# Optimization experiments

Hardware: AMD Instinct MI355X
Metric: run time of the kernel (lower is better)

Reference implementation:

```python
import jax, jax.numpy as jnp
import numpy as np

B, NF, EMB = 2048, 32, 64
FEAT_MAP_DIM = [128, 128, 128]  # split_half=True, activation=None


def setup_inputs() -> dict:
    key = jax.random.key(0)
    ks = jax.random.split(key, 7)
    inp = jax.random.normal(ks[0], (B, NF, EMB), dtype=jnp.float32)
    # conv1d_i: in_channels = H_{i-1} * NF, out_channels = FEAT_MAP_DIM[i]
    # H_0 = NF = 32; H_1 = H_2 = 128 // 2 = 64 (split_half)
    in_chs = [NF * NF, (FEAT_MAP_DIM[0] // 2) * NF, (FEAT_MAP_DIM[1] // 2) * NF]
    params = {}
    for i, (ic, oc) in enumerate(zip(in_chs, FEAT_MAP_DIM)):
        bound = 1.0 / np.sqrt(ic)  # torch Conv1d default init range
        params[f"W{i}"] = jax.random.uniform(ks[1 + 2 * i], (oc, ic), jnp.float32, -bound, bound)
        params[f"b{i}"] = jax.random.uniform(ks[2 + 2 * i], (oc,), jnp.float32, -bound, bound)
    return {"inp": inp, **params}


def reference(inp, W0, b0, W1, b1, W2, b2):
    # CIN: h_k[b,o,e] = sum_{j,z} W_k[o, j*NF+z] * h_{k-1}[b,j,e] * inp[b,z,e] + b_k[o]
    # The torch code materializes the outer product then applies a 1x1 conv;
    # the fused triple einsum below computes identical math.
    nf = inp.shape[1]
    Ws, bs = [W0, W1, W2], [b0, b1, b2]
    h = inp
    outs = []
    n_layers = len(Ws)
    for i, (W, b) in enumerate(zip(Ws, bs)):
        O, Hj = W.shape[0], h.shape[1]
        Wr = W.reshape(O, Hj, nf)  # channel index c = j*nf + z
        nxt = jnp.einsum('bjk,bzk,ojz->bok', h, inp, Wr) + b[None, :, None]
        if i != n_layers - 1:  # split_half
            h, o = nxt[:, : O // 2], nxt[:, O // 2 :]
        else:
            o = nxt
        outs.append(o)
    out = jnp.concatenate(outs, axis=1)  # (B, 64+64+128, EMB)
    return jnp.sum(out, axis=2)  # (B, 256)
```

## Files before the change

### kernel.cpp

```cpp
#include <hip/hip_runtime.h>


typedef _Float16 f16;
typedef _Float16 f16x4 __attribute__((ext_vector_type(4)));
typedef _Float16 f16x8 __attribute__((ext_vector_type(8)));
typedef float f32x4 __attribute__((ext_vector_type(4)));
typedef float f32x16 __attribute__((ext_vector_type(16)));

#define HSTR 72
#define PBS  5120

__device__ __forceinline__ f32x16 zero16() {
    f32x16 v;
#pragma unroll
    for (int i = 0; i < 16; ++i) v[i] = 0.0f;
    return v;
}

__global__ void __launch_bounds__(256)
prep_frag(const float* __restrict__ W0, const float* __restrict__ W1,
          const float* __restrict__ W2, f16* __restrict__ dst)
{
    int g = (blockIdx.x * 256 + threadIdx.x) * 8;
    const float* src; int base, KK, rbase;
    if (g < 65536)       { src = W0; base = 0;      KK = 64;  rbase = 0;  }
    else if (g < 131072) { src = W0; base = 65536;  KK = 64;  rbase = 64; }
    else if (g < 262144) { src = W1; base = 131072; KK = 128; rbase = 0;  }
    else if (g < 393216) { src = W1; base = 262144; KK = 128; rbase = 64; }
    else                 { src = W2; base = 393216; KK = 128; rbase = 0;  }
    int local = g - base;
    int frag  = local >> 9;
    int lane  = (local >> 3) & 63;
    int kk    = frag % KK;
    int mc    = frag / KK;
    int row   = rbase + mc * 32 + (lane & 31);
    int col   = kk * 16 + (lane >> 5) * 8;
    int IC    = KK * 16;
    const float* s = src + (size_t)row * IC + col;
    f16x8 o;
#pragma unroll
    for (int i = 0; i < 8; ++i) o[i] = (f16)s[i];
    *(f16x8*)(dst + g) = o;
}

__device__ __forceinline__ void p_chunk(const f16* __restrict__ hrows,
                                        const f16x8 (&pB)[4],
                                        f16* __restrict__ pdst, int t, int q)
{
    f32x16 acc = zero16();
#pragma unroll
    for (int s = 0; s < 4; ++s) {
        f16x8 a = *(const f16x8*)(hrows + t * HSTR + s * 16 + q * 8);
        acc = __builtin_amdgcn_mfma_f32_32x32x16_f16(a, pB[s], acc, 0, 0, 0);
    }
#pragma unroll
    for (int r = 0; r < 16; ++r) {
        int row = (r & 3) + 8 * (r >> 2) + 4 * q;
        pdst[row * 32 + t] = (f16)acc[r];
    }
}

template <int HJ>
__device__ __forceinline__ void h_gemm4(const f16* __restrict__ Hf,
                                        const f16* __restrict__ h0,
                                        const f16* __restrict__ h1,
                                        int lane8, int t,
                                        const f16x8 (&ip)[2][2][2],
                                        f32x16 (&acc)[2][2])
{
    acc[0][0] = zero16(); acc[0][1] = zero16();
    acc[1][0] = zero16(); acc[1][1] = zero16();
    const f16* Wp = Hf + lane8;
    f16x8 wf[2][2];
    f16   sc[2][4];
#pragma unroll
    for (int ph = 0; ph < 2; ++ph) {
        wf[ph][0] = *(const f16x8*)(Wp + (ph * 2 + 0) * 512);
        wf[ph][1] = *(const f16x8*)(Wp + (ph * 2 + 1) * 512);
        sc[ph][0] = h0[ph * HSTR + t];
        sc[ph][1] = h0[ph * HSTR + 32 + t];
        sc[ph][2] = h1[ph * HSTR + t];
        sc[ph][3] = h1[ph * HSTR + 32 + t];
    }
    for (int jj = 0; jj < HJ; jj += 2) {
#pragma unroll
        for (int ph = 0; ph < 2; ++ph) {
            f16x8 w0 = wf[ph][0], w1 = wf[ph][1];
            f16 s00 = sc[ph][0], s01 = sc[ph][1];
            f16 s10 = sc[ph][2], s11 = sc[ph][3];
            int jn = jj + ph + 2;
            if (jn > HJ - 1) jn = HJ - 1;
            wf[ph][0] = *(const f16x8*)(Wp + (jn * 2 + 0) * 512);
            wf[ph][1] = *(const f16x8*)(Wp + (jn * 2 + 1) * 512);
            sc[ph][0] = h0[jn * HSTR + t];
            sc[ph][1] = h0[jn * HSTR + 32 + t];
            sc[ph][2] = h1[jn * HSTR + t];
            sc[ph][3] = h1[jn * HSTR + 32 + t];
            acc[0][0] = __builtin_amdgcn_mfma_f32_32x32x16_f16(w0, ip[0][0][0] * s00, acc[0][0], 0, 0, 0);
            acc[0][0] = __builtin_amdgcn_mfma_f32_32x32x16_f16(w1, ip[0][1][0] * s00, acc[0][0], 0, 0, 0);
            acc[0][1] = __builtin_amdgcn_mfma_f32_32x32x16_f16(w0, ip[0][0][1] * s01, acc[0][1], 0, 0, 0);
            acc[0][1] = __builtin_amdgcn_mfma_f32_32x32x16_f16(w1, ip[0][1][1] * s01, acc[0][1], 0, 0, 0);
            acc[1][0] = __builtin_amdgcn_mfma_f32_32x32x16_f16(w0, ip[1][0][0] * s10, acc[1][0], 0, 0, 0);
            acc[1][0] = __builtin_amdgcn_mfma_f32_32x32x16_f16(w1, ip[1][1][0] * s10, acc[1][0], 0, 0, 0);
            acc[1][1] = __builtin_amdgcn_mfma_f32_32x32x16_f16(w0, ip[1][0][1] * s11, acc[1][1], 0, 0, 0);
            acc[1][1] = __builtin_amdgcn_mfma_f32_32x32x16_f16(w1, ip[1][1][1] * s11, acc[1][1], 0, 0, 0);
        }
    }
}

__device__ __forceinline__ void load_bias(const float* __restrict__ bl,
                                          float (&bve)[16], int g, int q)
{
#pragma unroll
    for (int r = 0; r < 16; ++r)
        bve[r] = bl[g * 32 + (r & 3) + 8 * (r >> 2) + 4 * q];
}

__device__ __forceinline__ void epi4(const f32x16 (&acc)[2][2],
                                     f16* __restrict__ h0d, f16* __restrict__ h1d,
                                     const float (&bve)[16], int g, int t, int q)
{
#pragma unroll
    for (int r = 0; r < 16; ++r) {
        int row = g * 32 + (r & 3) + 8 * (r >> 2) + 4 * q;
        h0d[row * HSTR + t]      = (f16)(acc[0][0][r] + bve[r]);
        h0d[row * HSTR + 32 + t] = (f16)(acc[0][1][r] + bve[r]);
        h1d[row * HSTR + t]      = (f16)(acc[1][0][r] + bve[r]);
        h1d[row * HSTR + 32 + t] = (f16)(acc[1][1][r] + bve[r]);
    }
}

__global__ void __launch_bounds__(256, 2)
cin_h(const float* __restrict__ inp, const f16* __restrict__ Wf,
      f16* __restrict__ pW,
      const float* __restrict__ b0v, const float* __restrict__ b1v)
{
    __shared__ __attribute__((aligned(16))) f16 hL[4 * 64 * HSTR];

    const int tid   = threadIdx.x;
    const int w     = tid >> 6;
    const int lane  = tid & 63;
    const int t     = lane & 31;
    const int q     = lane >> 5;
    const int lane8 = lane * 8;
    const int bp    = w & 1;
    const int g     = w >> 1;
    const int b0i   = blockIdx.x * 4;

#pragma unroll
    for (int it = 0; it < 8; ++it) {
        int idx = it * 1024 + tid * 4;
        int b = idx >> 11, rem = idx & 2047;
        int z = rem >> 6, k = rem & 63;
        f32x4 v = *(const f32x4*)(inp + (size_t)(b0i + b) * 2048 + rem);
        f16x4 h4;
        h4[0] = (f16)v[0]; h4[1] = (f16)v[1]; h4[2] = (f16)v[2]; h4[3] = (f16)v[3];
        *(f16x4*)(hL + b * 64 * HSTR + z * HSTR + k) = h4;
    }
    __syncthreads();

    f16x8 ip[2][2][2];
#pragma unroll
    for (int b = 0; b < 2; ++b) {
        const f16* src = hL + (bp * 2 + b) * 64 * HSTR;
#pragma unroll
        for (int kq = 0; kq < 2; ++kq)
#pragma unroll
            for (int nh = 0; nh < 2; ++nh) {
                f16x8 v;
#pragma unroll
                for (int i = 0; i < 8; ++i)
                    v[i] = src[(kq * 16 + q * 8 + i) * HSTR + nh * 32 + t];
                ip[b][kq][nh] = v;
            }
    }
    f16x8 pB[4];
#pragma unroll
    for (int s = 0; s < 4; ++s)
        pB[s] = *(const f16x8*)(hL + w * 64 * HSTR + t * HSTR + s * 16 + q * 8);

    f16* pMy = pW + (size_t)(b0i + w) * PBS;
    const f16* H0 = Wf;
    const f16* H1 = Wf + 131072;
    f16* hA = hL + (bp * 2) * 64 * HSTR;
    f16* hB = hL + (bp * 2 + 1) * 64 * HSTR;
    f32x16 acc[2][2];
    float bve[16];

    p_chunk(hL + w * 64 * HSTR, pB, pMy, t, q);
    h_gemm4<32>(H0 + g * 64 * 512, hA, hB, lane8, t, ip, acc);
    load_bias(b0v, bve, g, q);
    __syncthreads();
    epi4(acc, hA, hB, bve, g, t, q);
    __syncthreads();

    p_chunk(hL + w * 64 * HSTR,             pB, pMy + 1024, t, q);
    p_chunk(hL + w * 64 * HSTR + 32 * HSTR, pB, pMy + 2048, t, q);
    h_gemm4<64>(H1 + g * 128 * 512, hA, hB, lane8, t, ip, acc);
    load_bias(b1v, bve, g, q);
    __syncthreads();
    epi4(acc, hA, hB, bve, g, t, q);
    __syncthreads();

    p_chunk(hL + w * 64 * HSTR,             pB, pMy + 3072, t, q);
    p_chunk(hL + w * 64 * HSTR + 32 * HSTR, pB, pMy + 4096, t, q);
}

template <int S>
__device__ __forceinline__ void o_tile(const f16* __restrict__ Of,
                                       const f16* __restrict__ pBase,
                                       const float* __restrict__ biasp,
                                       float* __restrict__ out,
                                       float* __restrict__ rP,
                                       int bg, int colbase, int tid)
{
    const int w = tid >> 6, lane = tid & 63, t = lane & 31, q = lane >> 5;
    const int lane8 = lane * 8;
    const int mi = w & 1, ki = w >> 1;
    const f16* Ap = Of + (size_t)(mi * 2 * S + ki * S) * 512 + lane8;
    const f16* Bp = pBase + (size_t)(bg * 32 + t) * PBS + ki * S * 16 + q * 8;

    f32x16 acc = zero16();
    f16x8 af[4], bf[4];
#pragma unroll
    for (int i = 0; i < 4; ++i) {
        af[i] = *(const f16x8*)(Ap + i * 512);
        bf[i] = *(const f16x8*)(Bp + i * 16);
    }
#pragma unroll 4
    for (int s = 0; s < S; ++s) {
        int idx = s & 3;
        f16x8 a = af[idx], b = bf[idx];
        int sn = s + 4 < S ? s + 4 : S - 1;
        af[idx] = *(const f16x8*)(Ap + sn * 512);
        bf[idx] = *(const f16x8*)(Bp + sn * 16);
        acc = __builtin_amdgcn_mfma_f32_32x32x16_f16(a, b, acc, 0, 0, 0);
    }
#pragma unroll
    for (int r = 0; r < 16; ++r) {
        int m = mi * 32 + (r & 3) + 8 * (r >> 2) + 4 * q;
        rP[(ki * 32 + t) * 64 + m] = acc[r];
    }
    __syncthreads();
#pragma unroll
    for (int it = 0; it < 2; ++it) {
        int idx4 = (it * 256 + tid) * 4;
        int n = idx4 >> 6, o = idx4 & 63;
        f32x4 v0 = *(const f32x4*)(rP + n * 64 + o);
        f32x4 v1 = *(const f32x4*)(rP + (32 + n) * 64 + o);
        f32x4 bb = *(const f32x4*)(biasp + o);
        f32x4 ov;
        ov[0] = v0[0] + v1[0] + 64.0f * bb[0];
        ov[1] = v0[1] + v1[1] + 64.0f * bb[1];
        ov[2] = v0[2] + v1[2] + 64.0f * bb[2];
        ov[3] = v0[3] + v1[3] + 64.0f * bb[3];
        *(f32x4*)(out + (size_t)(bg * 32 + n) * 256 + colbase + o) = ov;
    }
}

__global__ void __launch_bounds__(256, 2)
cin_out(const f16* __restrict__ Wf, const f16* __restrict__ pW,
        const float* __restrict__ b0v, const float* __restrict__ b1v,
        const float* __restrict__ b2v, float* __restrict__ out)
{
    __shared__ __attribute__((aligned(16))) float rP[2 * 32 * 64];
    const int tid = threadIdx.x;
    const int r  = blockIdx.x & 3;
    const int bg = blockIdx.x >> 2;
    if (r == 0)
        o_tile<32>(Wf + 65536,  pW,        b0v + 64, out, rP, bg, 0,   tid);
    else if (r == 1)
        o_tile<64>(Wf + 262144, pW + 1024, b1v + 64, out, rP, bg, 64,  tid);
    else if (r == 2)
        o_tile<64>(Wf + 393216, pW + 3072, b2v,      out, rP, bg, 128, tid);
    else
        o_tile<64>(Wf + 524288, pW + 3072, b2v + 64, out, rP, bg, 192, tid);
}

extern "C" void kernel_launch(void* const* d_in, const int* in_sizes, int n_in,
                              void* d_out, int out_size, void* d_ws, size_t ws_size,
                              hipStream_t stream)
{
    const float* inp = (const float*)d_in[0];
    const float* W0  = (const float*)d_in[1];
    const float* b0  = (const float*)d_in[2];
    const float* W1  = (const float*)d_in[3];
    const float* b1  = (const float*)d_in[4];
    const float* W2  = (const float*)d_in[5];
    const float* b2  = (const float*)d_in[6];
    float* out = (float*)d_out;

    f16* Wf = (f16*)d_ws;
    f16* pW = Wf + 655360;

    prep_frag<<<320, 256, 0, stream>>>(W0, W1, W2, Wf);
    cin_h<<<512, 256, 0, stream>>>(inp, Wf, pW, b0, b1);
    cin_out<<<256, 256, 0, stream>>>(Wf, pW, b0, b1, b2, out);
}
```

Baseline: 138.3 us.

## Stage weight fragments into LDS asynchronously and split output GEMM into 32-column tiles

The h-layer GEMM now streams weight fragments through a per-wave 4-slot LDS ring using global_load_lds with vmcnt waits, instead of register prefetch from global. This is meant to hide global latency and free registers. The output kernel is retiled so each block computes a 32-column slice with a 4-way K split across waves, doubling the grid to 512 blocks for better occupancy. It adds 32KB of shared memory per cin_h block, which may limit occupancy. The hand-written vmcnt counts must match the outstanding loads exactly, or the ring reads stale data.

```diff
diff --git a/kernel.cpp b/kernel.cpp
--- a/kernel.cpp
+++ b/kernel.cpp
@@ -16,6 +16,14 @@
     for (int i = 0; i < 16; ++i) v[i] = 0.0f;
     return v;
 }
+
+__device__ __forceinline__ void cp1k(const f16* g, f16* l) {
+    __builtin_amdgcn_global_load_lds(
+        (__attribute__((address_space(1))) void*)(unsigned long long)g,
+        (__attribute__((address_space(3))) void*)(unsigned int)(unsigned long long)l,
+        16, 0, 0);
+}
+#define WAITV(n) asm volatile("s_waitcnt vmcnt(" #n ")" ::: "memory")
 
 __global__ void __launch_bounds__(256)
 prep_frag(const float* __restrict__ W0, const float* __restrict__ W1,
@@ -60,52 +68,62 @@
     }
 }
 
+__device__ __forceinline__ void stage_j(const f16* __restrict__ Wg, int j,
+                                        f16* __restrict__ ring, int lane8)
+{
+    f16* slot = ring + (j & 3) * 1024;
+    const f16* gp = Wg + j * 1024 + lane8;
+    cp1k(gp, slot);
+    cp1k(gp + 512, slot + 512);
+}
+
+__device__ __forceinline__ void consume_j(const f16* __restrict__ ring, int j,
+                                          const f16* __restrict__ h0,
+                                          const f16* __restrict__ h1,
+                                          int lane8, int t,
+                                          const f16x8 (&ip)[2][2][2],
+                                          f32x16 (&acc)[2][2])
+{
+    const f16* slot = ring + (j & 3) * 1024;
+    f16x8 w0 = *(const f16x8*)(slot + lane8);
+    f16x8 w1 = *(const f16x8*)(slot + 512 + lane8);
+    f16 s00 = h0[j * HSTR + t];
+    f16 s01 = h0[j * HSTR + 32 + t];
+    f16 s10 = h1[j * HSTR + t];
+    f16 s11 = h1[j * HSTR + 32 + t];
+    acc[0][0] = __builtin_amdgcn_mfma_f32_32x32x16_f16(w0, ip[0][0][0] * s00, acc[0][0], 0, 0, 0);
+    acc[0][1] = __builtin_amdgcn_mfma_f32_32x32x16_f16(w0, ip[0][0][1] * s01, acc[0][1], 0, 0, 0);
+    acc[1][0] = __builtin_amdgcn_mfma_f32_32x32x16_f16(w0, ip[1][0][0] * s10, acc[1][0], 0, 0, 0);
+    acc[1][1] = __builtin_amdgcn_mfma_f32_32x32x16_f16(w0, ip[1][0][1] * s11, acc[1][1], 0, 0, 0);
+    acc[0][0] = __builtin_amdgcn_mfma_f32_32x32x16_f16(w1, ip[0][1][0] * s00, acc[0][0], 0, 0, 0);
+    acc[0][1] = __builtin_amdgcn_mfma_f32_32x32x16_f16(w1, ip[0][1][1] * s01, acc[0][1], 0, 0, 0);
+    acc[1][0] = __builtin_amdgcn_mfma_f32_32x32x16_f16(w1, ip[1][1][0] * s10, acc[1][0], 0, 0, 0);
+    acc[1][1] = __builtin_amdgcn_mfma_f32_32x32x16_f16(w1, ip[1][1][1] * s11, acc[1][1], 0, 0, 0);
+}
+
 template <int HJ>
-__device__ __forceinline__ void h_gemm4(const f16* __restrict__ Hf,
-                                        const f16* __restrict__ h0,
-                                        const f16* __restrict__ h1,
-                                        int lane8, int t,
-                                        const f16x8 (&ip)[2][2][2],
-                                        f32x16 (&acc)[2][2])
+__device__ __forceinline__ void h_gemm_async(const f16* __restrict__ Wg,
+                                             const f16* __restrict__ h0,
+                                             const f16* __restrict__ h1,
+                                             f16* __restrict__ ring,
+                                             int lane8, int t,
+                                             const f16x8 (&ip)[2][2][2],
+                                             f32x16 (&acc)[2][2])
 {
     acc[0][0] = zero16(); acc[0][1] = zero16();
     acc[1][0] = zero16(); acc[1][1] = zero16();
-    const f16* Wp = Hf + lane8;
-    f16x8 wf[2][2];
-    f16   sc[2][4];
-#pragma unroll
-    for (int ph = 0; ph < 2; ++ph) {
-        wf[ph][0] = *(const f16x8*)(Wp + (ph * 2 + 0) * 512);
-        wf[ph][1] = *(const f16x8*)(Wp + (ph * 2 + 1) * 512);
-        sc[ph][0] = h0[ph * HSTR + t];
-        sc[ph][1] = h0[ph * HSTR + 32 + t];
-        sc[ph][2] = h1[ph * HSTR + t];
-        sc[ph][3] = h1[ph * HSTR + 32 + t];
-    }
-    for (int jj = 0; jj < HJ; jj += 2) {
-#pragma unroll
-        for (int ph = 0; ph < 2; ++ph) {
-            f16x8 w0 = wf[ph][0], w1 = wf[ph][1];
-            f16 s00 = sc[ph][0], s01 = sc[ph][1];
-            f16 s10 = sc[ph][2], s11 = sc[ph][3];
-            int jn = jj + ph + 2;
-            if (jn > HJ - 1) jn = HJ - 1;
-            wf[ph][0] = *(const f16x8*)(Wp + (jn * 2 + 0) * 512);
-            wf[ph][1] = *(const f16x8*)(Wp + (jn * 2 + 1) * 512);
-            sc[ph][0] = h0[jn * HSTR + t];
-            sc[ph][1] = h0[jn * HSTR + 32 + t];
-            sc[ph][2] = h1[jn * HSTR + t];
-            sc[ph][3] = h1[jn * HSTR + 32 + t];
-            acc[0][0] = __builtin_amdgcn_mfma_f32_32x32x16_f16(w0, ip[0][0][0] * s00, acc[0][0], 0, 0, 0);
-            acc[0][0] = __builtin_amdgcn_mfma_f32_32x32x16_f16(w1, ip[0][1][0] * s00, acc[0][0], 0, 0, 0);
-            acc[0][1] = __builtin_amdgcn_mfma_f32_32x32x16_f16(w0, ip[0][0][1] * s01, acc[0][1], 0, 0, 0);
-            acc[0][1] = __builtin_amdgcn_mfma_f32_32x32x16_f16(w1, ip[0][1][1] * s01, acc[0][1], 0, 0, 0);
-            acc[1][0] = __builtin_amdgcn_mfma_f32_32x32x16_f16(w0, ip[1][0][0] * s10, acc[1][0], 0, 0, 0);
-            acc[1][0] = __builtin_amdgcn_mfma_f32_32x32x16_f16(w1, ip[1][1][0] * s10, acc[1][0], 0, 0, 0);
-            acc[1][1] = __builtin_amdgcn_mfma_f32_32x32x16_f16(w0, ip[1][0][1] * s11, acc[1][1], 0, 0, 0);
-            acc[1][1] = __builtin_amdgcn_mfma_f32_32x32x16_f16(w1, ip[1][1][1] * s11, acc[1][1], 0, 0, 0);
-        }
-    }
+    WAITV(0);
+    stage_j(Wg, 0, ring, lane8);
+    stage_j(Wg, 1, ring, lane8);
+    stage_j(Wg, 2, ring, lane8);
+    for (int j = 0; j < HJ - 3; ++j) {
+        WAITV(4);
+        stage_j(Wg, j + 3, ring, lane8);
+        consume_j(ring, j, h0, h1, lane8, t, ip, acc);
+    }
+    WAITV(4); consume_j(ring, HJ - 3, h0, h1, lane8, t, ip, acc);
+    WAITV(2); consume_j(ring, HJ - 2, h0, h1, lane8, t, ip, acc);
+    WAITV(0); consume_j(ring, HJ - 1, h0, h1, lane8, t, ip, acc);
 }
 
 __device__ __forceinline__ void load_bias(const float* __restrict__ bl,
@@ -136,6 +154,7 @@
       const float* __restrict__ b0v, const float* __restrict__ b1v)
 {
     __shared__ __attribute__((aligned(16))) f16 hL[4 * 64 * HSTR];
+    __shared__ __attribute__((aligned(16))) f16 ringS[4][4096];
 
     const int tid   = threadIdx.x;
     const int w     = tid >> 6;
@@ -146,6 +165,7 @@
     const int bp    = w & 1;
     const int g     = w >> 1;
     const int b0i   = blockIdx.x * 4;
+    f16* ring = ringS[w];
 
 #pragma unroll
     for (int it = 0; it < 8; ++it) {
@@ -188,7 +208,7 @@
     float bve[16];
 
     p_chunk(hL + w * 64 * HSTR, pB, pMy, t, q);
-    h_gemm4<32>(H0 + g * 64 * 512, hA, hB, lane8, t, ip, acc);
+    h_gemm_async<32>(H0 + g * 64 * 512, hA, hB, ring, lane8, t, ip, acc);
     load_bias(b0v, bve, g, q);
     __syncthreads();
     epi4(acc, hA, hB, bve, g, t, q);
@@ -196,7 +216,7 @@
 
     p_chunk(hL + w * 64 * HSTR,             pB, pMy + 1024, t, q);
     p_chunk(hL + w * 64 * HSTR + 32 * HSTR, pB, pMy + 2048, t, q);
-    h_gemm4<64>(H1 + g * 128 * 512, hA, hB, lane8, t, ip, acc);
+    h_gemm_async<64>(H1 + g * 128 * 512, hA, hB, ring, lane8, t, ip, acc);
     load_bias(b1v, bve, g, q);
     __syncthreads();
     epi4(acc, hA, hB, bve, g, t, q);
@@ -206,55 +226,56 @@
     p_chunk(hL + w * 64 * HSTR + 32 * HSTR, pB, pMy + 4096, t, q);
 }
 
-template <int S>
-__device__ __forceinline__ void o_tile(const f16* __restrict__ Of,
-                                       const f16* __restrict__ pBase,
-                                       const float* __restrict__ biasp,
-                                       float* __restrict__ out,
-                                       float* __restrict__ rP,
-                                       int bg, int colbase, int tid)
-{
+template <int KK>
+__device__ __forceinline__ void o_tile32(const f16* __restrict__ Om,
+                                         const f16* __restrict__ pBase,
+                                         const float* __restrict__ biasp,
+                                         float* __restrict__ out,
+                                         float* __restrict__ rP,
+                                         int bg, int colbase, int tid)
+{
+    constexpr int S = KK / 4;
     const int w = tid >> 6, lane = tid & 63, t = lane & 31, q = lane >> 5;
     const int lane8 = lane * 8;
-    const int mi = w & 1, ki = w >> 1;
-    const f16* Ap = Of + (size_t)(mi * 2 * S + ki * S) * 512 + lane8;
-    const f16* Bp = pBase + (size_t)(bg * 32 + t) * PBS + ki * S * 16 + q * 8;
+    const f16* Ap = Om + (size_t)(w * S) * 512 + lane8;
+    const f16* Bp = pBase + (size_t)(bg * 32 + t) * PBS + w * S * 16 + q * 8;
 
     f32x16 acc = zero16();
-    f16x8 af[4], bf[4];
-#pragma unroll
-    for (int i = 0; i < 4; ++i) {
+    f16x8 af[8], bf[8];
+#pragma unroll
+    for (int i = 0; i < 8; ++i) {
         af[i] = *(const f16x8*)(Ap + i * 512);
         bf[i] = *(const f16x8*)(Bp + i * 16);
     }
-#pragma unroll 4
+#pragma unroll 8
     for (int s = 0; s < S; ++s) {
-        int idx = s & 3;
+        int idx = s & 7;
         f16x8 a = af[idx], b = bf[idx];
-        int sn = s + 4 < S ? s + 4 : S - 1;
+        int sn = s + 8 < S ? s + 8 : S - 1;
         af[idx] = *(const f16x8*)(Ap + sn * 512);
         bf[idx] = *(const f16x8*)(Bp + sn * 16);
         acc = __builtin_amdgcn_mfma_f32_32x32x16_f16(a, b, acc, 0, 0, 0);
     }
 #pragma unroll
     for (int r = 0; r < 16; ++r) {
-        int m = mi * 32 + (r & 3) + 8 * (r >> 2) + 4 * q;
-        rP[(ki * 32 + t) * 64 + m] = acc[r];
-    }
-    __syncthreads();
-#pragma unroll
-    for (int it = 0; it < 2; ++it) {
-        int idx4 = (it * 256 + tid) * 4;
-        int n = idx4 >> 6, o = idx4 & 63;
-        f32x4 v0 = *(const f32x4*)(rP + n * 64 + o);
-        f32x4 v1 = *(const f32x4*)(rP + (32 + n) * 64 + o);
-        f32x4 bb = *(const f32x4*)(biasp + o);
+        int m = (r & 3) + 8 * (r >> 2) + 4 * q;
+        rP[(w * 32 + t) * 32 + m] = acc[r];
+    }
+    __syncthreads();
+    {
+        int n  = tid >> 3;
+        int o4 = (tid & 7) * 4;
+        f32x4 v0 = *(const f32x4*)(rP + (0 * 32 + n) * 32 + o4);
+        f32x4 v1 = *(const f32x4*)(rP + (1 * 32 + n) * 32 + o4);
+        f32x4 v2 = *(const f32x4*)(rP + (2 * 32 + n) * 32 + o4);
+        f32x4 v3 = *(const f32x4*)(rP + (3 * 32 + n) * 32 + o4);
+        f32x4 bb = *(const f32x4*)(biasp + o4);
         f32x4 ov;
-        ov[0] = v0[0] + v1[0] + 64.0f * bb[0];
-        ov[1] = v0[1] + v1[1] + 64.0f * bb[1];
-        ov[2] = v0[2] + v1[2] + 64.0f * bb[2];
-        ov[3] = v0[3] + v1[3] + 64.0f * bb[3];
-        *(f32x4*)(out + (size_t)(bg * 32 + n) * 256 + colbase + o) = ov;
+        ov[0] = v0[0] + v1[0] + v2[0] + v3[0] + 64.0f * bb[0];
+        ov[1] = v0[1] + v1[1] + v2[1] + v3[1] + 64.0f * bb[1];
+        ov[2] = v0[2] + v1[2] + v2[2] + v3[2] + 64.0f * bb[2];
+        ov[3] = v0[3] + v1[3] + v2[3] + v3[3] + 64.0f * bb[3];
+        *(f32x4*)(out + (size_t)(bg * 32 + n) * 256 + colbase + o4) = ov;
     }
 }
 
@@ -263,18 +284,19 @@
         const float* __restrict__ b0v, const float* __restrict__ b1v,
         const float* __restrict__ b2v, float* __restrict__ out)
 {
-    __shared__ __attribute__((aligned(16))) float rP[2 * 32 * 64];
+    __shared__ __attribute__((aligned(16))) float rP[4 * 32 * 32];
     const int tid = threadIdx.x;
-    const int r  = blockIdx.x & 3;
-    const int bg = blockIdx.x >> 2;
-    if (r == 0)
-        o_tile<32>(Wf + 65536,  pW,        b0v + 64, out, rP, bg, 0,   tid);
-    else if (r == 1)
-        o_tile<64>(Wf + 262144, pW + 1024, b1v + 64, out, rP, bg, 64,  tid);
-    else if (r == 2)
-        o_tile<64>(Wf + 393216, pW + 3072, b2v,      out, rP, bg, 128, tid);
+    const int r  = blockIdx.x & 7;
+    const int bg = blockIdx.x >> 3;
+    if (r < 2)
+        o_tile32<64>(Wf + 65536 + r * 64 * 512, pW, b0v + 64 + r * 32,
+                     out, rP, bg, r * 32, tid);
+    else if (r < 4)
+        o_tile32<128>(Wf + 262144 + (r - 2) * 128 * 512, pW + 1024,
+                      b1v + 64 + (r - 2) * 32, out, rP, bg, 64 + (r - 2) * 32, tid);
     else
-        o_tile<64>(Wf + 524288, pW + 3072, b2v + 64, out, rP, bg, 192, tid);
+        o_tile32<128>(Wf + 393216 + (r - 4) * 128 * 512, pW + 3072,
+                      b2v + (r - 4) * 32, out, rP, bg, 128 + (r - 4) * 32, tid);
 }
 
 extern "C" void kernel_launch(void* const* d_in, const int* in_sizes, int n_in,
@@ -295,5 +317,5 @@
 
     prep_frag<<<320, 256, 0, stream>>>(W0, W1, W2, Wf);
     cin_h<<<512, 256, 0, stream>>>(inp, Wf, pW, b0, b1);
-    cin_out<<<256, 256, 0, stream>>>(Wf, pW, b0, b1, b2, out);
-}
+    cin_out<<<512, 256, 0, stream>>>(Wf, pW, b0, b1, b2, out);
+}
```

After: 141.6 us. 2.4% more time.
